# Performance work log

Hardware: AMD Instinct MI355X
Metric: run time of the kernel (lower is better)

Reference implementation:

```python
import jax, jax.numpy as jnp
import numpy as np

B, N, D = 1, 4301, 768          # batch, tokens (4200 patch + 1 cls + 100 det), dim
H, HD = 12, 64                  # heads, head_dim (all_head_dim = 768)
NDET = 100                      # det tokens at the end of the sequence
EPS = 1e-5                      # torch LayerNorm default eps
SCALE = HD ** -0.5


def setup_inputs() -> dict:
    key = jax.random.key(0)
    ks = jax.random.split(key, 10)
    w = lambda k: jax.random.normal(k, (D, D), dtype=jnp.float32) * 0.02
    return {
        "x": jax.random.normal(ks[0], (B, N, D), dtype=jnp.float32),
        "wq_p": w(ks[1]), "wk_p": w(ks[2]), "wv_p": w(ks[3]),
        "wq_d": w(ks[4]), "wk_d": w(ks[5]), "wv_d": w(ks[6]),
        "bq_p": jnp.zeros((D,), jnp.float32), "bv_p": jnp.zeros((D,), jnp.float32),
        "bq_d": jnp.zeros((D,), jnp.float32), "bv_d": jnp.zeros((D,), jnp.float32),
        "ln_g": jnp.ones((D,), jnp.float32), "ln_b": jnp.zeros((D,), jnp.float32),
        "wo_p": w(ks[7]), "bo_p": jnp.zeros((D,), jnp.float32),
        "wo_d": w(ks[8]), "bo_d": jnp.zeros((D,), jnp.float32),
    }


def reference(x, wq_p, wk_p, wv_p, wq_d, wk_d, wv_d,
              bq_p, bv_p, bq_d, bv_d, ln_g, ln_b,
              wo_p, bo_p, wo_d, bo_d):
    xp = x[:, :-NDET, :]                       # [B, N-100, D] patch (+cls) tokens
    xd = x[:, -NDET:, :]                       # [B, 100, D]   det tokens
    # separate patch/det QKV projections (subln=True path; k has no bias)
    q = jnp.concatenate([xp @ wq_p.T + bq_p, xd @ wq_d.T + bq_d], axis=1)
    k = jnp.concatenate([xp @ wk_p.T,        xd @ wk_d.T],        axis=1)
    v = jnp.concatenate([xp @ wv_p.T + bv_p, xd @ wv_d.T + bv_d], axis=1)
    split = lambda t: t.reshape(B, N, H, HD).transpose(0, 2, 1, 3)  # [B,H,N,HD]
    q, k, v = split(q) * SCALE, split(k), split(v)
    # unfused attention (memory_efficient_attention_pytorch, attn_mask=None)
    attn = jax.nn.softmax(jnp.einsum("bhqd,bhkd->bhqk", q, k), axis=-1)
    o = jnp.einsum("bhqk,bhkd->bhqd", attn, v)
    o = o.transpose(0, 2, 1, 3).reshape(B, N, D)
    # inner_attn_ln (LayerNorm over all_head_dim)
    mu = o.mean(-1, keepdims=True)
    var = ((o - mu) ** 2).mean(-1, keepdims=True)
    o = (o - mu) * jax.lax.rsqrt(var + EPS) * ln_g + ln_b
    # separate patch/det output projections
    out = jnp.concatenate([o[:, :-NDET, :] @ wo_p.T + bo_p,
                           o[:, -NDET:, :] @ wo_d.T + bo_d], axis=1)
    return out
```

## Files before the change

### kernel.cpp

```cpp
#include <hip/hip_runtime.h>
#include <hip/hip_bf16.h>

#define NT 4301
#define NP 4201
#define NDET 100
#define DMODEL 768
#define NHEAD 12
#define HD 64
#define LN_EPS 1e-5f
#define LOG2E 1.4426950408889634f
#define QSCALE (0.125f * LOG2E)
#define NTP 4352
#define NCHUNK 68
#define FRAGSZ 512
#define CHUNKSZ 4096

typedef __hip_bfloat16 bf16;
typedef __attribute__((ext_vector_type(4))) float f32x4;
typedef __attribute__((ext_vector_type(8))) short frag8;
typedef __attribute__((ext_vector_type(2))) unsigned int u32x2;

static __device__ __forceinline__ void permlane32_swap(unsigned& a, unsigned& b) {
#if __has_builtin(__builtin_amdgcn_permlane32_swap)
    u32x2 r = __builtin_amdgcn_permlane32_swap(a, b, false, false);
    a = r[0]; b = r[1];
#else
    asm("v_permlane32_swap_b32 %0, %1" : "+v"(a), "+v"(b));
#endif
}
static __device__ __forceinline__ void permlane16_swap(unsigned& a, unsigned& b) {
#if __has_builtin(__builtin_amdgcn_permlane16_swap)
    u32x2 r = __builtin_amdgcn_permlane16_swap(a, b, false, false);
    a = r[0]; b = r[1];
#else
    asm("v_permlane16_swap_b32 %0, %1" : "+v"(a), "+v"(b));
#endif
}

static __device__ __forceinline__ unsigned pack_bf16_rh(float a, float b) {
    unsigned ua = __builtin_bit_cast(unsigned, a) + 0x8000u;
    unsigned ub = __builtin_bit_cast(unsigned, b) + 0x8000u;
    return __builtin_amdgcn_perm(ub, ua, 0x07060302u);
}

__global__ __launch_bounds__(256) void cast_all_kernel(
    const float* __restrict__ x,
    const float* __restrict__ w0, const float* __restrict__ w1,
    const float* __restrict__ w2, const float* __restrict__ w3,
    const float* __restrict__ w4, const float* __restrict__ w5,
    const float* __restrict__ w6, const float* __restrict__ w7,
    bf16* __restrict__ dst, int nx, int nw, int total) {
    int i4 = (blockIdx.x * 256 + threadIdx.x) * 4;
    if (i4 >= total) return;
    const float* s;
    int off;
    if (i4 < nx) {
        s = x; off = i4;
    } else {
        int r = i4 - nx;
        int w = r / nw;
        off = r - w * nw;
        s = w0;
        if (w == 1) s = w1; else if (w == 2) s = w2; else if (w == 3) s = w3;
        else if (w == 4) s = w4; else if (w == 5) s = w5;
        else if (w == 6) s = w6; else if (w == 7) s = w7;
    }
    float4 v = *(const float4*)(s + off);
    bf16 o[4] = {__float2bfloat16(v.x), __float2bfloat16(v.y),
                 __float2bfloat16(v.z), __float2bfloat16(v.w)};
    *(ushort4*)(dst + i4) = *(ushort4*)o;
}

__global__ __launch_bounds__(256, 4) void qkv_kernel(
    const bf16* __restrict__ xb, const bf16* __restrict__ wbase,
    const float* __restrict__ bq_p, const float* __restrict__ bq_d,
    const float* __restrict__ bv_p, const float* __restrict__ bv_d,
    bf16* __restrict__ Qb, bf16* __restrict__ Ksw, bf16* __restrict__ Vsw) {
    __shared__ bf16 As[64][32];
    __shared__ bf16 Bs[192][32];

    const int tid = threadIdx.x;
    const int wave = tid >> 6, lane = tid & 63;
    const int quad = lane >> 4, l16 = lane & 15;
    const int bx = blockIdx.x;
    const int h = blockIdx.y;
    const int is_det = bx >= 66;
    const int row0 = is_det ? NP + (bx - 66) * 64 : bx * 64;
    const int Mlim = is_det ? NT : NP;
    const int col0 = h * 64;
    const size_t nw = (size_t)DMODEL * DMODEL;
    const bf16* W = wbase + (is_det ? 3 * nw : 0);

    const f32x4 z4 = {0.f, 0.f, 0.f, 0.f};
    f32x4 acc[4][3];
#pragma unroll
    for (int r4 = 0; r4 < 4; ++r4)
#pragma unroll
        for (int f = 0; f < 3; ++f) acc[r4][f] = z4;

    const int srow = tid >> 2;
    const int scol8 = (tid & 3) * 8;
    int a_r = row0 + srow;
    if (a_r >= Mlim) a_r = Mlim - 1;
    const bf16* ap = xb + (size_t)a_r * DMODEL + scol8;
    const bf16* bp = W + (size_t)(col0 + srow) * DMODEL + scol8;

    uint4 areg  = *(const uint4*)(ap);
    uint4 breg0 = *(const uint4*)(bp);
    uint4 breg1 = *(const uint4*)(bp + nw);
    uint4 breg2 = *(const uint4*)(bp + 2 * nw);

    for (int k0 = 0; k0 < DMODEL; k0 += 32) {
        __syncthreads();
        *(uint4*)(&As[srow][scol8]) = areg;
        *(uint4*)(&Bs[srow][scol8]) = breg0;
        *(uint4*)(&Bs[64 + srow][scol8]) = breg1;
        *(uint4*)(&Bs[128 + srow][scol8]) = breg2;
        if (k0 + 32 < DMODEL) {
            areg  = *(const uint4*)(ap + k0 + 32);
            breg0 = *(const uint4*)(bp + k0 + 32);
            breg1 = *(const uint4*)(bp + nw + k0 + 32);
            breg2 = *(const uint4*)(bp + 2 * nw + k0 + 32);
        }
        __asm__ volatile("s_waitcnt lgkmcnt(0)" ::: "memory");
        __builtin_amdgcn_s_barrier();
        __asm__ volatile("" ::: "memory");
        frag8 af[4], bfr[3];
#pragma unroll
        for (int r4 = 0; r4 < 4; ++r4)
            af[r4] = *(const frag8*)(&As[r4 * 16 + l16][quad * 8]);
#pragma unroll
        for (int f = 0; f < 3; ++f)
            bfr[f] = *(const frag8*)(&Bs[wave * 48 + f * 16 + l16][quad * 8]);
#pragma unroll
        for (int r4 = 0; r4 < 4; ++r4)
#pragma unroll
            for (int f = 0; f < 3; ++f)
                acc[r4][f] = __builtin_amdgcn_mfma_f32_16x16x32_bf16(af[r4], bfr[f], acc[r4][f], 0, 0, 0);
        __asm__ volatile("" ::: "memory");
    }

#pragma unroll
    for (int f = 0; f < 3; ++f) {
        const int oc = 3 * wave + f;
        const int opi = oc >> 2;
        const int cin = (oc & 3) * 16 + l16;
        const int c = col0 + cin;
        float bv = 0.f, scale = 1.f;
        if (opi == 0) { bv = (is_det ? bq_d : bq_p)[c]; scale = QSCALE; }
        else if (opi == 2) { bv = (is_det ? bv_d : bv_p)[c]; }
#pragma unroll
        for (int r4 = 0; r4 < 4; ++r4) {
#pragma unroll
            for (int j = 0; j < 4; ++j) {
                const int r = row0 + r4 * 16 + quad * 4 + j;
                if (r >= Mlim) continue;
                const bf16 val = __float2bfloat16((acc[r4][f][j] + bv) * scale);
                if (opi == 0) {
                    Qb[(size_t)r * DMODEL + c] = val;
                } else if (opi == 1) {
                    const int cc = r >> 6, tf = (r >> 4) & 3, ln = r & 15;
                    const int s = cin >> 5, qd = (cin >> 3) & 3, je = cin & 7;
                    Ksw[((size_t)(h * NCHUNK + cc) * 8 + tf * 2 + s) * FRAGSZ +
                        (qd * 16 + ln) * 8 + je] = val;
                } else {
                    const int t = cin >> 4, le = cin & 15;
                    const int cc = r >> 6, rr = r & 63;
                    const int sv = rr >> 5, qv = (rr >> 3) & 3, je = rr & 7;
                    Vsw[((size_t)(h * NCHUNK + cc) * 8 + t * 2 + sv) * FRAGSZ +
                        (qv * 16 + le) * 8 + je] = val;
                }
            }
        }
    }
}

__global__ __launch_bounds__(256, 2) void attn_kernel(
    const bf16* __restrict__ Q, const bf16* __restrict__ Ksw,
    const bf16* __restrict__ Vsw, float* __restrict__ O_part,
    float* __restrict__ l_part, int cpb) {
    const int tid = threadIdx.x;
    const int wave = tid >> 6, lane = tid & 63;
    const int quad = lane >> 4, l16 = lane & 15;
    const int h = blockIdx.y;
    const int z = blockIdx.z;
    const int qbase = blockIdx.x * 128;
    const int hoff = h * HD;
    const int c0 = z * cpb, c1 = c0 + cpb;

    frag8 ones;
#pragma unroll
    for (int j = 0; j < 8; ++j) ones[j] = (short)0x3F80;

    frag8 qf[2][2];
#pragma unroll
    for (int g = 0; g < 2; ++g) {
        int qr = qbase + wave * 32 + g * 16 + l16;
        if (qr >= NT) qr = NT - 1;
#pragma unroll
        for (int s = 0; s < 2; ++s)
            qf[g][s] = *(const frag8*)(Q + (size_t)qr * DMODEL + hoff + s * 32 + quad * 8);
    }

    const bf16* kb0 = Ksw + (size_t)h * NCHUNK * CHUNKSZ + lane * 8;
    const bf16* vb0 = Vsw + (size_t)h * NCHUNK * CHUNKSZ + lane * 8;

    const f32x4 z4 = {0.f, 0.f, 0.f, 0.f};
    f32x4 accO[2][4], accL[2];
#pragma unroll
    for (int g = 0; g < 2; ++g) {
        accL[g] = z4;
#pragma unroll
        for (int t = 0; t < 4; ++t) accO[g][t] = z4;
    }

    for (int c = c0; c < c1; ++c) {
        const bf16* kc = kb0 + (size_t)c * CHUNKSZ;
        const bf16* vc = vb0 + (size_t)c * CHUNKSZ;
        frag8 kf[8], vf[8];
#pragma unroll
        for (int f = 0; f < 8; ++f) {
            kf[f] = *(const frag8*)(kc + f * FRAGSZ);
            vf[f] = *(const frag8*)(vc + f * FRAGSZ);
        }

        f32x4 S[2][4];
#pragma unroll
        for (int g = 0; g < 2; ++g)
#pragma unroll
            for (int t = 0; t < 4; ++t) {
                f32x4 s0 = __builtin_amdgcn_mfma_f32_16x16x32_bf16(kf[t * 2 + 0], qf[g][0], z4, 0, 0, 0);
                S[g][t]  = __builtin_amdgcn_mfma_f32_16x16x32_bf16(kf[t * 2 + 1], qf[g][1], s0, 0, 0, 0);
            }
        if (c == NCHUNK - 1) {
            const int kb = c * 64 + quad * 4;
#pragma unroll
            for (int t = 0; t < 4; ++t)
#pragma unroll
                for (int j = 0; j < 4; ++j)
                    if (kb + t * 16 + j >= NT) {
                        S[0][t][j] = -1e30f;
                        S[1][t][j] = -1e30f;
                    }
        }

#pragma unroll
        for (int g = 0; g < 2; ++g) {
            unsigned lo[4], hi[4];
#pragma unroll
            for (int t = 0; t < 4; ++t) {
                lo[t] = pack_bf16_rh(__builtin_exp2f(S[g][t][0]),
                                     __builtin_exp2f(S[g][t][1]));
                hi[t] = pack_bf16_rh(__builtin_exp2f(S[g][t][2]),
                                     __builtin_exp2f(S[g][t][3]));
            }
#pragma unroll
            for (int s = 0; s < 2; ++s) {
                unsigned A = lo[2 * s], B = hi[2 * s];
                unsigned C = lo[2 * s + 1], D = hi[2 * s + 1];
                permlane32_swap(A, C);
                permlane32_swap(B, D);
                permlane16_swap(A, C);
                permlane16_swap(B, D);
                union { unsigned u[4]; frag8 f; } pu;
                pu.u[0] = A; pu.u[1] = B; pu.u[2] = C; pu.u[3] = D;
                const frag8 pf = pu.f;
                accL[g] = __builtin_amdgcn_mfma_f32_16x16x32_bf16(pf, ones, accL[g], 0, 0, 0);
#pragma unroll
                for (int t = 0; t < 4; ++t)
                    accO[g][t] = __builtin_amdgcn_mfma_f32_16x16x32_bf16(pf, vf[t * 2 + s], accO[g][t], 0, 0, 0);
            }
        }
    }

    float* Op = O_part + (size_t)z * NT * DMODEL;
#pragma unroll
    for (int g = 0; g < 2; ++g)
#pragma unroll
        for (int j = 0; j < 4; ++j) {
            const int r = qbase + wave * 32 + g * 16 + quad * 4 + j;
            if (r < NT) {
#pragma unroll
                for (int t = 0; t < 4; ++t)
                    Op[(size_t)r * DMODEL + hoff + t * 16 + l16] = accO[g][t][j];
                if (l16 == 0)
                    l_part[((size_t)z * NHEAD + h) * NTP + r] = accL[g][j];
            }
        }
}

__global__ __launch_bounds__(192) void reduce_ln_kernel(
    const float* __restrict__ O_part, const float* __restrict__ l_part,
    const float* __restrict__ g, const float* __restrict__ b,
    bf16* __restrict__ out, int nsplit) {
    const int n = blockIdx.x;
    const int tid = threadIdx.x;
    const int d0 = tid * 4;
    const int hh = d0 >> 6;

    float4 o = make_float4(0.f, 0.f, 0.f, 0.f);
    float lv = 0.f;
    for (int s = 0; s < nsplit; ++s) {
        float4 v = *(const float4*)(O_part + ((size_t)s * NT + n) * DMODEL + d0);
        o.x += v.x; o.y += v.y; o.z += v.z; o.w += v.w;
        lv += l_part[((size_t)s * NHEAD + hh) * NTP + n];
    }
    const float inv_l = 1.0f / lv;
    float vals[4] = {o.x * inv_l, o.y * inv_l, o.z * inv_l, o.w * inv_l};

    float s = vals[0] + vals[1] + vals[2] + vals[3];
    float s2 = vals[0] * vals[0] + vals[1] * vals[1] + vals[2] * vals[2] + vals[3] * vals[3];
#pragma unroll
    for (int off = 1; off < 64; off <<= 1) {
        s += __shfl_xor(s, off);
        s2 += __shfl_xor(s2, off);
    }
    __shared__ float ss[3], ss2[3];
    const int wave = tid >> 6, lane = tid & 63;
    if (lane == 0) { ss[wave] = s; ss2[wave] = s2; }
    __syncthreads();
    s = ss[0] + ss[1] + ss[2];
    s2 = ss2[0] + ss2[1] + ss2[2];
    const float mu = s * (1.0f / 768.0f);
    float var = s2 * (1.0f / 768.0f) - mu * mu;
    const float inv = rsqrtf(var + LN_EPS);

    unsigned short pk[4];
#pragma unroll
    for (int i = 0; i < 4; ++i) {
        const int d = d0 + i;
        const float v = (vals[i] - mu) * inv * g[d] + b[d];
        bf16 bb = __float2bfloat16(v);
        pk[i] = *(unsigned short*)&bb;
    }
    *(ushort4*)(out + (size_t)n * DMODEL + d0) = *(ushort4*)pk;
}

__global__ __launch_bounds__(256, 2) void out_kernel(
    const bf16* __restrict__ Lb, const bf16* __restrict__ wo,
    const float* __restrict__ bo_p, const float* __restrict__ bo_d,
    float* __restrict__ out) {
    __shared__ bf16 As[128][32];
    __shared__ bf16 Bs[64][32];

    const int tid = threadIdx.x;
    const int wave = tid >> 6, lane = tid & 63;
    const int quad = lane >> 4, l16 = lane & 15;
    const int bx = blockIdx.x;
    const int is_det = bx >= 33;
    const int row0 = is_det ? NP : bx * 128;
    const int Mlim = is_det ? NT : NP;
    const int col0 = blockIdx.y * 64;
    const size_t nw = (size_t)DMODEL * DMODEL;
    const bf16* B = wo + (is_det ? nw : 0);
    const float* bias = is_det ? bo_d : bo_p;

    const f32x4 z4 = {0.f, 0.f, 0.f, 0.f};
    f32x4 acc[2][4];
#pragma unroll
    for (int gg = 0; gg < 2; ++gg)
#pragma unroll
        for (int t = 0; t < 4; ++t) acc[gg][t] = z4;

    const int arow = tid >> 1;
    const int acol = (tid & 1) * 16;
    int a_r = row0 + arow;
    if (a_r >= Mlim) a_r = Mlim - 1;
    const bf16* ap = Lb + (size_t)a_r * DMODEL + acol;
    const int brow = tid >> 2;
    const int bcol = (tid & 3) * 8;
    const bf16* bp = B + (size_t)(col0 + brow) * DMODEL + bcol;

    uint4 areg0 = *(const uint4*)(ap);
    uint4 areg1 = *(const uint4*)(ap + 8);
    uint4 breg  = *(const uint4*)(bp);

    for (int k0 = 0; k0 < DMODEL; k0 += 32) {
        __syncthreads();
        *(uint4*)(&As[arow][acol]) = areg0;
        *(uint4*)(&As[arow][acol + 8]) = areg1;
        *(uint4*)(&Bs[brow][bcol]) = breg;
        if (k0 + 32 < DMODEL) {
            areg0 = *(const uint4*)(ap + k0 + 32);
            areg1 = *(const uint4*)(ap + k0 + 40);
            breg  = *(const uint4*)(bp + k0 + 32);
        }
        __asm__ volatile("s_waitcnt lgkmcnt(0)" ::: "memory");
        __builtin_amdgcn_s_barrier();
        __asm__ volatile("" ::: "memory");
        frag8 af[2], bfq[4];
#pragma unroll
        for (int gg = 0; gg < 2; ++gg)
            af[gg] = *(const frag8*)(&As[wave * 32 + gg * 16 + l16][quad * 8]);
#pragma unroll
        for (int t = 0; t < 4; ++t)
            bfq[t] = *(const frag8*)(&Bs[t * 16 + l16][quad * 8]);
#pragma unroll
        for (int gg = 0; gg < 2; ++gg)
#pragma unroll
            for (int t = 0; t < 4; ++t)
                acc[gg][t] = __builtin_amdgcn_mfma_f32_16x16x32_bf16(af[gg], bfq[t], acc[gg][t], 0, 0, 0);
        __asm__ volatile("" ::: "memory");
    }

#pragma unroll
    for (int gg = 0; gg < 2; ++gg) {
        const int rbase = row0 + wave * 32 + gg * 16 + quad * 4;
#pragma unroll
        for (int t = 0; t < 4; ++t) {
            const int c = col0 + t * 16 + l16;
            const float bv = bias[c];
#pragma unroll
            for (int j = 0; j < 4; ++j) {
                const int r = rbase + j;
                if (r < Mlim) out[(size_t)r * DMODEL + c] = acc[gg][t][j] + bv;
            }
        }
    }
}

extern "C" void kernel_launch(void* const* d_in, const int* in_sizes, int n_in,
                              void* d_out, int out_size, void* d_ws, size_t ws_size,
                              hipStream_t stream) {
    const float* x    = (const float*)d_in[0];
    const float* wq_p = (const float*)d_in[1];
    const float* wk_p = (const float*)d_in[2];
    const float* wv_p = (const float*)d_in[3];
    const float* wq_d = (const float*)d_in[4];
    const float* wk_d = (const float*)d_in[5];
    const float* wv_d = (const float*)d_in[6];
    const float* bq_p = (const float*)d_in[7];
    const float* bv_p = (const float*)d_in[8];
    const float* bq_d = (const float*)d_in[9];
    const float* bv_d = (const float*)d_in[10];
    const float* ln_g = (const float*)d_in[11];
    const float* ln_b = (const float*)d_in[12];
    const float* wo_p = (const float*)d_in[13];
    const float* bo_p = (const float*)d_in[14];
    const float* wo_d = (const float*)d_in[15];
    const float* bo_d = (const float*)d_in[16];
    float* out = (float*)d_out;

    const size_t nx  = (size_t)NT * DMODEL;
    const size_t nsw = (size_t)NHEAD * NCHUNK * CHUNKSZ;
    const size_t nw  = (size_t)DMODEL * DMODEL;

    char* ws = (char*)d_ws;
    bf16* xb   = (bf16*)ws; ws += nx * 2;
    bf16* wqkv = (bf16*)ws; ws += 6 * nw * 2;
    bf16* wob  = (bf16*)ws; ws += 2 * nw * 2;
    bf16* Qb   = (bf16*)ws; ws += nx * 2;
    bf16* Ksw  = (bf16*)ws; ws += nsw * 2;
    bf16* Vsw  = (bf16*)ws; ws += nsw * 2;
    const size_t fixed = (size_t)(ws - (char*)d_ws);

    const size_t per_split = nx * 4 + (size_t)NHEAD * NTP * 4;
    int nsplit = 1;
    if (ws_size >= fixed + 4 * per_split) nsplit = 4;
    else if (ws_size >= fixed + 2 * per_split) nsplit = 2;
    const int cpb = NCHUNK / nsplit;

    float* O_part = (float*)ws;
    float* l_part = (float*)(ws + (size_t)nsplit * nx * 4);
    bf16* Lb = xb;

    const int total = (int)(nx + 8 * nw);
    cast_all_kernel<<<dim3((total / 4 + 255) / 256), dim3(256), 0, stream>>>(
        x, wq_p, wk_p, wv_p, wq_d, wk_d, wv_d, wo_p, wo_d, xb, (int)nx, (int)nw, total);

    qkv_kernel<<<dim3(68, 12), dim3(256), 0, stream>>>(
        xb, wqkv, bq_p, bq_d, bv_p, bv_d, Qb, Ksw, Vsw);

    attn_kernel<<<dim3(34, NHEAD, nsplit), dim3(256), 0, stream>>>(
        Qb, Ksw, Vsw, O_part, l_part, cpb);

    reduce_ln_kernel<<<dim3(NT), dim3(192), 0, stream>>>(
        O_part, l_part, ln_g, ln_b, Lb, nsplit);

    out_kernel<<<dim3(34, 12), dim3(256), 0, stream>>>(Lb, wob, bo_p, bo_d, out);
}
```

Measured before the change: 263.0 us.

## Double-buffer K/V chunks in LDS via async global_load_lds and XCD-aware block mapping

Instead of each wave loading the whole K/V chunk from global memory into registers, the four waves cooperatively stream each chunk into a double-buffered LDS tile using direct global-to-LDS loads, prefetching the next chunk while the current one is computed. The grid becomes 1D and is remapped so that blocks sharing a head and split land on the same XCD, which should improve L2 reuse of K/V. This cuts redundant global traffic and hides load latency, at the cost of two barriers per chunk, extra LDS use, and hand-written waitcnt logic that could hurt occupancy.

New measurement: 266.2 us. About the same (+1.2%).

```diff
diff --git a/kernel.cpp b/kernel.cpp
--- a/kernel.cpp
+++ b/kernel.cpp
@@ -41,6 +41,12 @@
     unsigned ua = __builtin_bit_cast(unsigned, a) + 0x8000u;
     unsigned ub = __builtin_bit_cast(unsigned, b) + 0x8000u;
     return __builtin_amdgcn_perm(ub, ua, 0x07060302u);
+}
+
+static __device__ __forceinline__ void gload16(const bf16* g, bf16* l) {
+    __builtin_amdgcn_global_load_lds(
+        (const __attribute__((address_space(1))) void*)g,
+        (__attribute__((address_space(3))) void*)l, 16, 0, 0);
 }
 
 __global__ __launch_bounds__(256) void cast_all_kernel(
@@ -179,12 +185,28 @@
     const bf16* __restrict__ Q, const bf16* __restrict__ Ksw,
     const bf16* __restrict__ Vsw, float* __restrict__ O_part,
     float* __restrict__ l_part, int cpb) {
+    __shared__ bf16 KV[2][16][FRAGSZ];
+
     const int tid = threadIdx.x;
     const int wave = tid >> 6, lane = tid & 63;
     const int quad = lane >> 4, l16 = lane & 15;
-    const int h = blockIdx.y;
-    const int z = blockIdx.z;
-    const int qbase = blockIdx.x * 128;
+
+    int bx, h, z;
+    {
+        const int id = blockIdx.x;
+        const int nblk = gridDim.x;
+        const int per = nblk >> 3;
+        if ((nblk & 7) == 0 && per % 34 == 0) {
+            const int ppx = per / 34;
+            const int q = id >> 3;
+            const int pair = (id & 7) * ppx + q / 34;
+            bx = q % 34;
+            h = pair % NHEAD; z = pair / NHEAD;
+        } else {
+            bx = id % 34; h = (id / 34) % NHEAD; z = id / (34 * NHEAD);
+        }
+    }
+    const int qbase = bx * 128;
     const int hoff = h * HD;
     const int c0 = z * cpb, c1 = c0 + cpb;
 
@@ -204,6 +226,9 @@
 
     const bf16* kb0 = Ksw + (size_t)h * NCHUNK * CHUNKSZ + lane * 8;
     const bf16* vb0 = Vsw + (size_t)h * NCHUNK * CHUNKSZ + lane * 8;
+    const bf16* sb = (wave < 2) ? kb0 : vb0;
+    const int foff = (wave & 1) * 4;
+    const int fbase = 4 * wave;
 
     const f32x4 z4 = {0.f, 0.f, 0.f, 0.f};
     f32x4 accO[2][4], accL[2];
@@ -214,14 +239,34 @@
         for (int t = 0; t < 4; ++t) accO[g][t] = z4;
     }
 
+    __asm__ volatile("s_waitcnt vmcnt(0)" ::: "memory");
+
+    {
+        const bf16* s = sb + (size_t)c0 * CHUNKSZ + foff * FRAGSZ;
+#pragma unroll
+        for (int i = 0; i < 4; ++i)
+            gload16(s + i * FRAGSZ, &KV[0][fbase + i][0]);
+    }
+
+    int p = 0;
     for (int c = c0; c < c1; ++c) {
-        const bf16* kc = kb0 + (size_t)c * CHUNKSZ;
-        const bf16* vc = vb0 + (size_t)c * CHUNKSZ;
+        if (c + 1 < c1) {
+            const bf16* s = sb + (size_t)(c + 1) * CHUNKSZ + foff * FRAGSZ;
+#pragma unroll
+            for (int i = 0; i < 4; ++i)
+                gload16(s + i * FRAGSZ, &KV[p ^ 1][fbase + i][0]);
+            __asm__ volatile("s_waitcnt vmcnt(4)" ::: "memory");
+        } else {
+            __asm__ volatile("s_waitcnt vmcnt(0)" ::: "memory");
+        }
+        __builtin_amdgcn_s_barrier();
+        __asm__ volatile("" ::: "memory");
+
         frag8 kf[8], vf[8];
 #pragma unroll
         for (int f = 0; f < 8; ++f) {
-            kf[f] = *(const frag8*)(kc + f * FRAGSZ);
-            vf[f] = *(const frag8*)(vc + f * FRAGSZ);
+            kf[f] = *(const frag8*)(&KV[p][f][lane * 8]);
+            vf[f] = *(const frag8*)(&KV[p][8 + f][lane * 8]);
         }
 
         f32x4 S[2][4];
@@ -271,6 +316,11 @@
                     accO[g][t] = __builtin_amdgcn_mfma_f32_16x16x32_bf16(pf, vf[t * 2 + s], accO[g][t], 0, 0, 0);
             }
         }
+
+        __asm__ volatile("s_waitcnt lgkmcnt(0)" ::: "memory");
+        __builtin_amdgcn_s_barrier();
+        __asm__ volatile("" ::: "memory");
+        p ^= 1;
     }
 
     float* Op = O_part + (size_t)z * NT * DMODEL;
@@ -471,7 +521,7 @@
     qkv_kernel<<<dim3(68, 12), dim3(256), 0, stream>>>(
         xb, wqkv, bq_p, bq_d, bv_p, bv_d, Qb, Ksw, Vsw);
 
-    attn_kernel<<<dim3(34, NHEAD, nsplit), dim3(256), 0, stream>>>(
+    attn_kernel<<<dim3(34 * NHEAD * nsplit), dim3(256), 0, stream>>>(
         Qb, Ksw, Vsw, O_part, l_part, cpb);
 
     reduce_ln_kernel<<<dim3(NT), dim3(192), 0, stream>>>(
```
